# Kernel optimization log

Measured on AMD Instinct MI355X. Metric: run time of the kernel, lower is better.

Reference implementation:

```python
import jax, jax.numpy as jnp
import numpy as np

N = 8000      # num_nodes
U = 64        # num_units
D = 2         # input_dim
K = 2         # max_diffusion_step
E = 64000     # edges per support
B = 32        # batch
F = D + U     # concat feature size = 66
M = 2 * K + 1 # num_matrices = 5


def setup_inputs() -> dict:
    key = jax.random.key(0)
    ks = jax.random.split(key, 10)
    return {
        "inputs": jax.random.normal(ks[0], (B, N * D), dtype=jnp.float32),
        "hx": jax.random.normal(ks[1], (B, N * U), dtype=jnp.float32),
        "row0": jax.random.randint(ks[2], (E,), 0, N, dtype=jnp.int32),
        "col0": jax.random.randint(ks[3], (E,), 0, N, dtype=jnp.int32),
        "val0": jax.random.uniform(ks[4], (E,), dtype=jnp.float32) / 8.0,
        "row1": jax.random.randint(ks[5], (E,), 0, N, dtype=jnp.int32),
        "col1": jax.random.randint(ks[6], (E,), 0, N, dtype=jnp.int32),
        "val1": jax.random.uniform(ks[7], (E,), dtype=jnp.float32) / 8.0,
        "W_ru": jax.random.normal(ks[8], (F * M, 2 * U), dtype=jnp.float32) * 0.05,
        "b_ru": jnp.ones((2 * U,), dtype=jnp.float32),  # bias_start=1.0
        "W_c": jax.random.normal(ks[9], (F * M, U), dtype=jnp.float32) * 0.05,
        "b_c": jnp.zeros((U,), dtype=jnp.float32),       # bias_start=0.0
    }


def _spmm(row, col, val, x):
    # y[r] += val_e * x[c]  for each edge e=(r,c); x: [N, F*B]
    return jax.ops.segment_sum(val[:, None] * x[col], row, num_segments=N)


def _gconv(inputs, state, W, b, supports, output_size):
    # inputs: [B, N*D_in], state: [B, N*D_st]
    x = jnp.concatenate([inputs.reshape(B, N, -1), state.reshape(B, N, -1)], axis=2)  # [B,N,F]
    f = x.shape[2]
    x0 = x.transpose(1, 2, 0).reshape(N, f * B)  # [N, F*B]
    xs = [x0]
    for (row, col, val) in supports:
        x1 = _spmm(row, col, val, x0)
        xs.append(x1)
        xk_1, xk_2 = x1, x0
        for _ in range(2, K + 1):
            x2 = 2.0 * _spmm(row, col, val, xk_1) - xk_2
            xs.append(x2)
            xk_1, xk_2 = x2, xk_1
    m = len(xs)
    # [M,N,F,B] -> [B,N,F,M] -> [B*N, F*M]
    xc = jnp.stack(xs).reshape(m, N, f, B).transpose(3, 1, 2, 0).reshape(B * N, f * m)
    out = xc @ W + b
    return out.reshape(B, N * output_size)


def reference(inputs, hx, row0, col0, val0, row1, col1, val1, W_ru, b_ru, W_c, b_c):
    supports = ((row0, col0, val0), (row1, col1, val1))
    # reset/update gates via graph convolution
    value = jax.nn.sigmoid(_gconv(inputs, hx, W_ru, b_ru, supports, 2 * U))
    value = value.reshape(B, N, 2 * U)
    r = value[..., :U].reshape(B, N * U)
    u = value[..., U:].reshape(B, N * U)
    c = jnp.tanh(_gconv(inputs, r * hx, W_c, b_c, supports, U))
    new_state = u * hx + (1.0 - u) * c
    return new_state
```

## Files before the change

kernel.cpp:

```cpp
#include <hip/hip_runtime.h>
#include <stdint.h>

#define NN 8000
#define UU 64
#define EE 64000
#define BB 32
#define NB 256000
#define HXS 512000

typedef __attribute__((ext_vector_type(8))) __bf16 bf16x8;
typedef __attribute__((ext_vector_type(4))) float f32x4;
typedef __attribute__((ext_vector_type(4))) unsigned int u32x4;

__device__ __forceinline__ unsigned short f2bf(float f){
  unsigned int u = __builtin_bit_cast(unsigned int, f);
  u += 0x7fffu + ((u >> 16) & 1u);
  return (unsigned short)(u >> 16);
}
__device__ __forceinline__ unsigned int pack2(float a, float b){
  return (unsigned int)f2bf(a) | ((unsigned int)f2bf(b) << 16);
}
__device__ __forceinline__ float bflo(unsigned int w){ return __builtin_bit_cast(float, w << 16); }
__device__ __forceinline__ float bfhi(unsigned int w){ return __builtin_bit_cast(float, w & 0xffff0000u); }
__device__ __forceinline__ float bfu(unsigned short v){ return __builtin_bit_cast(float, (unsigned int)v << 16); }

__device__ __forceinline__ void acc8(float* a, float v, uint4 q){
  a[0]+=v*bflo(q.x); a[1]+=v*bfhi(q.x); a[2]+=v*bflo(q.y); a[3]+=v*bfhi(q.y);
  a[4]+=v*bflo(q.z); a[5]+=v*bfhi(q.z); a[6]+=v*bflo(q.w); a[7]+=v*bfhi(q.w);
}

__device__ __forceinline__ void stage16(const unsigned short* g, unsigned short* ldsbase){
  __builtin_amdgcn_global_load_lds((const __attribute__((address_space(1))) void*)g,
                                   (__attribute__((address_space(3))) void*)ldsbase, 16, 0, 0);
}

__global__ void k_hist(const int* __restrict__ r0, const int* __restrict__ r1, int* __restrict__ cnt){
  int i = blockIdx.x * 256 + threadIdx.x;
  if (i < 2*EE){
    int s = (i >= EE);
    int r = s ? r1[i - EE] : r0[i];
    atomicAdd(&cnt[s*NN + r], 1);
  }
}

__global__ __launch_bounds__(1024) void k_scan(const int* __restrict__ cnt, int* __restrict__ row_ptr, int* __restrict__ rp_work){
  int sup = blockIdx.x;
  const int* c = cnt + sup*NN;
  __shared__ int part[1024];
  int t = threadIdx.x;
  int loc[8]; int s = 0;
  #pragma unroll
  for (int j=0;j<8;j++){ int idx=t*8+j; int v = (idx<NN)? c[idx]:0; loc[j]=s; s+=v; }
  part[t]=s; __syncthreads();
  for (int o=1;o<1024;o<<=1){
    int v = (t>=o)? part[t-o]:0;
    __syncthreads();
    part[t]+=v;
    __syncthreads();
  }
  int pre = (t>0)? part[t-1]:0;
  #pragma unroll
  for (int j=0;j<8;j++){ int idx=t*8+j; if(idx<NN){ int e=pre+loc[j]; row_ptr[sup*(NN+1)+idx]=e; rp_work[sup*NN+idx]=e; } }
  if (t==1023) row_ptr[sup*(NN+1)+NN] = part[1023];
}

__global__ void k_scatter(const int* __restrict__ r0, const int* __restrict__ c0, const float* __restrict__ v0,
                          const int* __restrict__ r1, const int* __restrict__ c1, const float* __restrict__ v1,
                          int* __restrict__ rp_work, int* __restrict__ col_s, float* __restrict__ val_s){
  int i = blockIdx.x * 256 + threadIdx.x;
  if (i < 2*EE){
    int s = (i >= EE);
    int e = s ? i - EE : i;
    int r  = s ? r1[e] : r0[e];
    int cc = s ? c1[e] : c0[e];
    float vv = s ? v1[e] : v0[e];
    int pos = atomicAdd(&rp_work[s*NN + r], 1);
    col_s[s*EE + pos] = cc;
    val_s[s*EE + pos] = vv;
  }
}

__global__ void k_wpack(const float* __restrict__ W_ru, const float* __restrict__ W_c,
                        unsigned short* __restrict__ Wru_t, unsigned short* __restrict__ Wc_t){
  int i = blockIdx.x * 256 + threadIdx.x;
  int k = i / 192; int oo = i % 192;
  const float* W; int ld, NC; unsigned short* dst; int c;
  if (oo < 128){ W = W_ru; ld = 128; NC = 128; dst = Wru_t; c = oo; }
  else         { W = W_c;  ld = 64;  NC = 64;  dst = Wc_t;  c = oo - 128; }
  int o = 4*(c & 15) + ((c >> 4) & 3);
  int wcol = (c >= 64) ? 64 + o : o;
  float v = 0.f;
  if (k < 330){
    int m, fb;
    if (k < 320){ m = k >> 6; fb = (2 + (k & 63)) * 5; }
    else        { int j = k - 320; m = j >> 1; fb = (j & 1) * 5; }
    if      (m==0) v = W[(fb+0)*ld+wcol] - W[(fb+2)*ld+wcol] - W[(fb+4)*ld+wcol];
    else if (m==1) v = W[(fb+1)*ld+wcol];
    else if (m==2) v = 2.f*W[(fb+2)*ld+wcol];
    else if (m==3) v = W[(fb+3)*ld+wcol];
    else           v = 2.f*W[(fb+4)*ld+wcol];
  }
  int dstoff;
  if (k < 320) dstoff = (k>>6)*NC*64 + c*64 + (k&63);
  else         dstoff = 320*NC + c*32 + (k-320);
  dst[dstoff] = f2bf(v);
}

__global__ void k_x0(const float* __restrict__ inputs, const float* __restrict__ hx,
                     uint4* __restrict__ xs0q, unsigned int* __restrict__ xi0){
  int n = blockIdx.x, t = threadIdx.x;
  int b = t >> 3, ug = t & 7;
  const float4 h0 = *(const float4*)(hx + (size_t)b*HXS + n*64 + ug*8);
  const float4 h1 = *(const float4*)(hx + (size_t)b*HXS + n*64 + ug*8 + 4);
  uint4 o;
  o.x = pack2(h0.x, h0.y); o.y = pack2(h0.z, h0.w);
  o.z = pack2(h1.x, h1.y); o.w = pack2(h1.z, h1.w);
  xs0q[(size_t)(b>>1)*(NN*16) + (size_t)n*16 + (b&1)*8 + ug] = o;
  if (t < 32){
    int bb = t;
    const float2 g = *(const float2*)(inputs + (size_t)bb*(NN*2) + n*2);
    xi0[(((size_t)(bb>>2)*NN) + n)*4 + (bb&3)] = pack2(g.x, g.y);
  }
}

template<bool WITH_IN, bool NTDST>
__global__ void k_spmm(const int* __restrict__ row_ptr, const int* __restrict__ col_s, const float* __restrict__ val_s,
                       uint4* xs4, uint4* xi4,
                       int srcA, int dstA, int srcB, int dstB){
  int bid = blockIdx.x;
  if (WITH_IN && bid >= 16000){
    int b2 = bid - 16000;
    int s = b2 & 7, supi = (b2 >> 3) & 1, chunk = b2 >> 4;
    int n = chunk*256 + threadIdx.x;
    if (n >= NN) return;
    int msrc = supi ? srcB : srcA, mdst = supi ? dstB : dstA;
    size_t sb = (size_t)(msrc*8 + s)*NN, db = (size_t)(mdst*8 + s)*NN;
    int beg = row_ptr[supi*(NN+1)+n], end = row_ptr[supi*(NN+1)+n+1];
    const int* cs = col_s + supi*EE; const float* vs = val_s + supi*EE;
    float ai[8] = {0.f,0.f,0.f,0.f,0.f,0.f,0.f,0.f};
    for (int e = beg; e < end; ++e){
      int c = cs[e]; float v = vs[e];
      uint4 qi = xi4[sb + c];
      acc8(ai, v, qi);
    }
    uint4 oi;
    oi.x = pack2(ai[0],ai[1]); oi.y = pack2(ai[2],ai[3]); oi.z = pack2(ai[4],ai[5]); oi.w = pack2(ai[6],ai[7]);
    if (NTDST){
      u32x4 ov = {oi.x, oi.y, oi.z, oi.w};
      __builtin_nontemporal_store(ov, (u32x4*)&xi4[db + n]);
    } else xi4[db + n] = oi;
    return;
  }
  int xcd = bid & 7;
  int seq = bid >> 3;
  int supi = (seq >= 1000) ? 1 : 0;
  int seq2 = seq - supi*1000;
  int slice = (seq2 < 500) ? xcd : (xcd + 8);
  int group = (seq2 < 500) ? seq2 : (seq2 - 500);
  int sub = threadIdx.x >> 4, lane = threadIdx.x & 15;
  int n = group*16 + sub;
  int msrc = supi ? srcB : srcA, mdst = supi ? dstB : dstA;
  size_t sS = (size_t)msrc*(NN*256) + (size_t)slice*(NN*16);
  size_t dS = (size_t)mdst*(NN*256) + (size_t)slice*(NN*16);
  int beg = row_ptr[supi*(NN+1)+n], end = row_ptr[supi*(NN+1)+n+1];
  const int* cs = col_s + supi*EE;
  const float* vs = val_s + supi*EE;

  float a[8] = {0.f,0.f,0.f,0.f,0.f,0.f,0.f,0.f};
  int e = beg;
  for (; e + 4 <= end; e += 4){
    int c0=cs[e], c1=cs[e+1], c2=cs[e+2], c3=cs[e+3];
    float v0=vs[e], v1=vs[e+1], v2=vs[e+2], v3=vs[e+3];
    uint4 q0 = xs4[sS + (size_t)c0*16 + lane];
    uint4 q1 = xs4[sS + (size_t)c1*16 + lane];
    uint4 q2 = xs4[sS + (size_t)c2*16 + lane];
    uint4 q3 = xs4[sS + (size_t)c3*16 + lane];
    acc8(a, v0, q0); acc8(a, v1, q1); acc8(a, v2, q2); acc8(a, v3, q3);
  }
  for (; e < end; ++e){
    int c = cs[e]; float v = vs[e];
    uint4 q = xs4[sS + (size_t)c*16 + lane];
    acc8(a, v, q);
  }
  uint4 o;
  o.x = pack2(a[0],a[1]); o.y = pack2(a[2],a[3]); o.z = pack2(a[4],a[5]); o.w = pack2(a[6],a[7]);
  if (NTDST){
    u32x4 ov = {o.x, o.y, o.z, o.w};
    __builtin_nontemporal_store(ov, (u32x4*)&xs4[dS + (size_t)n*16 + lane]);
  } else xs4[dS + (size_t)n*16 + lane] = o;
}

template<int NCOL, bool IS_RU>
__global__ __launch_bounds__(256, 3) void k_gemm(unsigned short* xsS,
                                                 const unsigned int* __restrict__ xsI,
                                                 const unsigned short* __restrict__ Wp,
                                                 const float* __restrict__ bias,
                                                 const float* __restrict__ hx,
                                                 float* cout,
                                                 unsigned short* ubuf){
  constexpr int CF = NCOL / 16;
  __shared__ unsigned short Bl[2][NCOL*64];
  __shared__ unsigned short Bt[NCOL*32];
  const int t = threadIdx.x;
  const int wv = t >> 6;
  const int l = t & 63;
  const int lr = l & 15;
  const int lg = l >> 4;
  const int R0 = blockIdx.x * 128;

  auto stageB = [&](int m, int buf){
    #pragma unroll
    for (int i=0;i<NCOL*8/256;i++){
      int g = t + i*256;
      int rr = g >> 3, c = g & 7;
      const unsigned short* gp = Wp + (size_t)(m*NCOL + rr)*64 + ((c ^ (rr&7)) << 3);
      stage16(gp, &Bl[buf][(size_t)(i*256 + wv*64)*8]);
    }
  };

  size_t abase[2];
  #pragma unroll
  for (int rf=0; rf<2; rf++){
    int row = R0 + wv*32 + rf*16 + lr;
    int n = row >> 5, b = row & 31;
    abase[rf] = (size_t)(b>>1)*(NN*128) + (size_t)n*128 + (b&1)*64;
  }
  auto loadA = [&](int m, uint4* dst){
    #pragma unroll
    for (int ks=0; ks<2; ks++)
      #pragma unroll
      for (int rf=0; rf<2; rf++)
        dst[ks*2+rf] = *(const uint4*)(xsS + (size_t)m*(NN*2048) + abase[rf] + ks*32 + lg*8);
  };

  uint4 aC[4], aN[4];
  loadA(0, aC);
  uint4 aT[2];
  #pragma unroll
  for (int rf=0; rf<2; rf++){
    int row = R0 + wv*32 + rf*16 + lr;
    int n = row >> 5, b = row & 31;
    size_t ib = (((size_t)(b>>2))*NN + n)*4 + (b&3);
    unsigned int q0=0u,q1=0u,q2=0u,q3=0u;
    if (lg == 0){
      q0 = xsI[ib];
      q1 = xsI[(size_t)8*NN*4 + ib];
      q2 = xsI[(size_t)16*NN*4 + ib];
      q3 = xsI[(size_t)24*NN*4 + ib];
    } else if (lg == 1){
      q0 = xsI[(size_t)32*NN*4 + ib];
    }
    uint4 qq; qq.x=q0; qq.y=q1; qq.z=q2; qq.w=q3;
    aT[rf] = qq;
  }
  stageB(0, 0);
  {
    #pragma unroll
    for (int i=0;i<NCOL*4/256;i++){
      int g = t + i*256;
      int rr = g >> 2, c = g & 3;
      const unsigned short* gp = Wp + (size_t)320*NCOL + rr*32 + ((c ^ (rr&3)) << 3);
      stage16(gp, &Bt[(size_t)(i*256 + wv*64)*8]);
    }
  }
  __syncthreads();

  f32x4 acc[2][CF];
  const f32x4 zero = {0.f,0.f,0.f,0.f};
  #pragma unroll
  for (int rf=0; rf<2; rf++)
    #pragma unroll
    for (int cf=0; cf<CF; cf++) acc[rf][cf] = zero;

  #pragma unroll
  for (int m=0; m<5; m++){
    int cur = m & 1;
    if (m < 4){
      stageB(m+1, cur^1);
      loadA(m+1, aN);
    }
    #pragma unroll
    for (int ks=0; ks<2; ks++){
      #pragma unroll
      for (int cf=0; cf<CF; cf++){
        int col = cf*16 + lr;
        int chunk = (ks*4 + lg) ^ (col & 7);
        bf16x8 bv = __builtin_bit_cast(bf16x8, *(const uint4*)(&Bl[cur][col*64 + chunk*8]));
        acc[0][cf] = __builtin_amdgcn_mfma_f32_16x16x32_bf16(__builtin_bit_cast(bf16x8, aC[ks*2+0]), bv, acc[0][cf], 0, 0, 0);
        acc[1][cf] = __builtin_amdgcn_mfma_f32_16x16x32_bf16(__builtin_bit_cast(bf16x8, aC[ks*2+1]), bv, acc[1][cf], 0, 0, 0);
      }
    }
    __syncthreads();
    #pragma unroll
    for (int i=0;i<4;i++) aC[i] = aN[i];
  }

  #pragma unroll
  for (int cf=0; cf<CF; cf++){
    int col = cf*16 + lr;
    int chunk = lg ^ (col & 3);
    bf16x8 bv = __builtin_bit_cast(bf16x8, *(const uint4*)(&Bt[col*32 + chunk*8]));
    acc[0][cf] = __builtin_amdgcn_mfma_f32_16x16x32_bf16(__builtin_bit_cast(bf16x8, aT[0]), bv, acc[0][cf], 0, 0, 0);
    acc[1][cf] = __builtin_amdgcn_mfma_f32_16x16x32_bf16(__builtin_bit_cast(bf16x8, aT[1]), bv, acc[1][cf], 0, 0, 0);
  }

  #pragma unroll
  for (int rf=0; rf<2; rf++){
    #pragma unroll
    for (int reg=0; reg<4; reg++){
      int row = R0 + wv*32 + rf*16 + (lg << 2) + reg;
      int n = row >> 5, b = row & 31;
      size_t rowoff = (size_t)b*HXS + (size_t)n*UU;
      size_t slot0 = (size_t)(b>>1)*(NN*128) + (size_t)n*128 + (b&1)*64;
      int o0 = lr << 2;
      if constexpr (IS_RU){
        uint2 hv = *(const uint2*)(xsS + slot0 + o0);
        unsigned short rr4[4], uu4[4];
        #pragma unroll
        for (int cf=0; cf<4; cf++){
          int o = o0 + cf;
          float vr = acc[rf][cf][reg]   + bias[o];
          float vu = acc[rf][cf+4][reg] + bias[64+o];
          float sgr = 1.f/(1.f + __expf(-vr));
          float sgu = 1.f/(1.f + __expf(-vu));
          float h = bfu(((const unsigned short*)&hv)[cf]);
          rr4[cf] = f2bf(sgr * h);
          uu4[cf] = f2bf(sgu);
        }
        *(uint2*)(xsS + slot0 + o0) = *(uint2*)rr4;
        *(uint2*)(ubuf + rowoff + o0) = *(uint2*)uu4;
      } else {
        float4 hv = *(const float4*)(hx + rowoff + o0);
        uint2 uv = *(const uint2*)(ubuf + rowoff + o0);
        float4 ov;
        #pragma unroll
        for (int cf=0; cf<4; cf++){
          float cc = tanhf(acc[rf][cf][reg] + bias[o0+cf]);
          float uu = bfu(((const unsigned short*)&uv)[cf]);
          float h  = ((const float*)&hv)[cf];
          ((float*)&ov)[cf] = uu*h + (1.f - uu)*cc;
        }
        *(float4*)(cout + rowoff + o0) = ov;
      }
    }
  }
}

extern "C" void kernel_launch(void* const* d_in, const int* in_sizes, int n_in,
                              void* d_out, int out_size, void* d_ws, size_t ws_size,
                              hipStream_t stream){
  const float* inputs = (const float*)d_in[0];
  const float* hx     = (const float*)d_in[1];
  const int*   row0   = (const int*)d_in[2];
  const int*   col0   = (const int*)d_in[3];
  const float* val0   = (const float*)d_in[4];
  const int*   row1   = (const int*)d_in[5];
  const int*   col1   = (const int*)d_in[6];
  const float* val1   = (const float*)d_in[7];
  const float* W_ru   = (const float*)d_in[8];
  const float* b_ru   = (const float*)d_in[9];
  const float* W_c    = (const float*)d_in[10];
  const float* b_c    = (const float*)d_in[11];
  float* out = (float*)d_out;

  char* ws = (char*)d_ws;
  size_t off = 0;
  auto alloc = [&](size_t bytes) -> void* {
    void* p = ws + off;
    off += (bytes + 255) & ~(size_t)255;
    return p;
  };
  unsigned short* xsS   = (unsigned short*)alloc((size_t)5*NN*2048*2);
  unsigned int*   xsI   = (unsigned int*)  alloc((size_t)5*8*NN*16);
  unsigned short* u_buf = (unsigned short*)alloc((size_t)NB*64*2);
  unsigned short* Wru_t = (unsigned short*)alloc((size_t)128*352*2);
  unsigned short* Wc_t  = (unsigned short*)alloc((size_t)64*352*2);
  int*   row_ptr = (int*)  alloc(2*(NN+1)*4);
  int*   col_s   = (int*)  alloc(2*EE*4);
  float* val_s   = (float*)alloc(2*EE*4);
  int*   cnt     = (int*)  alloc(2*NN*4);
  int*   rp_work = (int*)  alloc(2*NN*4);
  (void)ws_size; (void)in_sizes; (void)n_in; (void)out_size;

  hipMemsetAsync(cnt, 0, 2*NN*4, stream);
  k_hist<<<(2*EE + 255)/256, 256, 0, stream>>>(row0, row1, cnt);
  k_scan<<<2, 1024, 0, stream>>>(cnt, row_ptr, rp_work);
  k_scatter<<<(2*EE + 255)/256, 256, 0, stream>>>(row0, col0, val0, row1, col1, val1, rp_work, col_s, val_s);
  k_wpack<<<(352*192)/256, 256, 0, stream>>>(W_ru, W_c, Wru_t, Wc_t);
  k_x0<<<NN, 256, 0, stream>>>(inputs, hx, (uint4*)xsS, (unsigned int*)xsI);

  uint4* xs4 = (uint4*)xsS;
  uint4* xi4 = (uint4*)xsI;

  k_spmm<true , false><<<16512, 256, 0, stream>>>(row_ptr, col_s, val_s, xs4, xi4, 0, 1, 0, 3);
  k_spmm<true , true ><<<16512, 256, 0, stream>>>(row_ptr, col_s, val_s, xs4, xi4, 1, 2, 3, 4);
  k_gemm<128, true><<<2000, 256, 0, stream>>>(xsS, xsI, Wru_t, b_ru, hx, nullptr, u_buf);

  k_spmm<false, false><<<16000, 256, 0, stream>>>(row_ptr, col_s, val_s, xs4, xi4, 0, 1, 0, 3);
  k_spmm<false, true ><<<16000, 256, 0, stream>>>(row_ptr, col_s, val_s, xs4, xi4, 1, 2, 3, 4);
  k_gemm<64, false><<<2000, 256, 0, stream>>>(xsS, xsI, Wc_t, b_c, hx, out, u_buf);
}
```

Baseline: 393.9 us.

## Preload all GEMM weights into LDS and stream A tiles via async LDS loads

The GEMM kernel now stages every weight slice (all five diffusion matrices plus the input tail) into shared memory up front. It streams activation fragments through a per-wave double-buffered LDS area using direct global-to-LDS loads with explicit vmcnt waits, replacing per-iteration block barriers. SpMM kernels drop the template flag and always write outputs with nontemporal stores. The larger shared-memory footprint lowers occupancy, and nontemporal stores on intermediate hops may hurt cache reuse by the following hop.

```diff
diff --git a/kernel.cpp b/kernel.cpp
--- a/kernel.cpp
+++ b/kernel.cpp
@@ -32,6 +32,11 @@
 __device__ __forceinline__ void stage16(const unsigned short* g, unsigned short* ldsbase){
   __builtin_amdgcn_global_load_lds((const __attribute__((address_space(1))) void*)g,
                                    (__attribute__((address_space(3))) void*)ldsbase, 16, 0, 0);
+}
+
+__device__ __forceinline__ void ntstore16(uint4 v, uint4* p){
+  u32x4 ov = {v.x, v.y, v.z, v.w};
+  __builtin_nontemporal_store(ov, (u32x4*)p);
 }
 
 __global__ void k_hist(const int* __restrict__ r0, const int* __restrict__ r1, int* __restrict__ cnt){
@@ -123,7 +128,7 @@
   }
 }
 
-template<bool WITH_IN, bool NTDST>
+template<bool WITH_IN>
 __global__ void k_spmm(const int* __restrict__ row_ptr, const int* __restrict__ col_s, const float* __restrict__ val_s,
                        uint4* xs4, uint4* xi4,
                        int srcA, int dstA, int srcB, int dstB){
@@ -145,10 +150,7 @@
     }
     uint4 oi;
     oi.x = pack2(ai[0],ai[1]); oi.y = pack2(ai[2],ai[3]); oi.z = pack2(ai[4],ai[5]); oi.w = pack2(ai[6],ai[7]);
-    if (NTDST){
-      u32x4 ov = {oi.x, oi.y, oi.z, oi.w};
-      __builtin_nontemporal_store(ov, (u32x4*)&xi4[db + n]);
-    } else xi4[db + n] = oi;
+    ntstore16(oi, &xi4[db + n]);
     return;
   }
   int xcd = bid & 7;
@@ -184,23 +186,24 @@
   }
   uint4 o;
   o.x = pack2(a[0],a[1]); o.y = pack2(a[2],a[3]); o.z = pack2(a[4],a[5]); o.w = pack2(a[6],a[7]);
-  if (NTDST){
-    u32x4 ov = {o.x, o.y, o.z, o.w};
-    __builtin_nontemporal_store(ov, (u32x4*)&xs4[dS + (size_t)n*16 + lane]);
-  } else xs4[dS + (size_t)n*16 + lane] = o;
+  ntstore16(o, &xs4[dS + (size_t)n*16 + lane]);
 }
 
 template<int NCOL, bool IS_RU>
-__global__ __launch_bounds__(256, 3) void k_gemm(unsigned short* xsS,
-                                                 const unsigned int* __restrict__ xsI,
-                                                 const unsigned short* __restrict__ Wp,
-                                                 const float* __restrict__ bias,
-                                                 const float* __restrict__ hx,
-                                                 float* cout,
-                                                 unsigned short* ubuf){
+__global__ __launch_bounds__(256) void k_gemm(unsigned short* xsS,
+                                              const unsigned int* __restrict__ xsI,
+                                              const unsigned short* __restrict__ Wp,
+                                              const float* __restrict__ bias,
+                                              const float* __restrict__ hx,
+                                              float* cout,
+                                              unsigned short* ubuf){
   constexpr int CF = NCOL / 16;
-  __shared__ unsigned short Bl[2][NCOL*64];
-  __shared__ unsigned short Bt[NCOL*32];
+  constexpr int BMAIN = 5*NCOL*64;
+  constexpr int BLD  = (5*NCOL*64/8)/256;
+  constexpr int BLDT = (NCOL*32/8)/256;
+  __shared__ unsigned short Bs[NCOL*352];
+  __shared__ unsigned short As[2][4][4][512];
+
   const int t = threadIdx.x;
   const int wv = t >> 6;
   const int l = t & 63;
@@ -208,16 +211,6 @@
   const int lg = l >> 4;
   const int R0 = blockIdx.x * 128;
 
-  auto stageB = [&](int m, int buf){
-    #pragma unroll
-    for (int i=0;i<NCOL*8/256;i++){
-      int g = t + i*256;
-      int rr = g >> 3, c = g & 7;
-      const unsigned short* gp = Wp + (size_t)(m*NCOL + rr)*64 + ((c ^ (rr&7)) << 3);
-      stage16(gp, &Bl[buf][(size_t)(i*256 + wv*64)*8]);
-    }
-  };
-
   size_t abase[2];
   #pragma unroll
   for (int rf=0; rf<2; rf++){
@@ -225,16 +218,7 @@
     int n = row >> 5, b = row & 31;
     abase[rf] = (size_t)(b>>1)*(NN*128) + (size_t)n*128 + (b&1)*64;
   }
-  auto loadA = [&](int m, uint4* dst){
-    #pragma unroll
-    for (int ks=0; ks<2; ks++)
-      #pragma unroll
-      for (int rf=0; rf<2; rf++)
-        dst[ks*2+rf] = *(const uint4*)(xsS + (size_t)m*(NN*2048) + abase[rf] + ks*32 + lg*8);
-  };
-
-  uint4 aC[4], aN[4];
-  loadA(0, aC);
+
   uint4 aT[2];
   #pragma unroll
   for (int rf=0; rf<2; rf++){
@@ -253,17 +237,30 @@
     uint4 qq; qq.x=q0; qq.y=q1; qq.z=q2; qq.w=q3;
     aT[rf] = qq;
   }
-  stageB(0, 0);
-  {
+  #pragma unroll
+  for (int i=0;i<BLD;i++){
+    int g = t + i*256;
+    int rr = g >> 3, c = g & 7;
+    const unsigned short* gp = Wp + (size_t)rr*64 + ((c ^ (rr&7)) << 3);
+    stage16(gp, &Bs[(size_t)(i*256 + wv*64)*8]);
+  }
+  #pragma unroll
+  for (int i=0;i<BLDT;i++){
+    int g = t + i*256;
+    int rr = g >> 2, c = g & 3;
+    const unsigned short* gp = Wp + (size_t)BMAIN + rr*32 + ((c ^ (rr&3)) << 3);
+    stage16(gp, &Bs[BMAIN + (size_t)(i*256 + wv*64)*8]);
+  }
+  auto stageA = [&](int m, int set){
     #pragma unroll
-    for (int i=0;i<NCOL*4/256;i++){
-      int g = t + i*256;
-      int rr = g >> 2, c = g & 3;
-      const unsigned short* gp = Wp + (size_t)320*NCOL + rr*32 + ((c ^ (rr&3)) << 3);
-      stage16(gp, &Bt[(size_t)(i*256 + wv*64)*8]);
+    for (int f=0; f<4; f++){
+      int ks = f >> 1, rf = f & 1;
+      const unsigned short* gp = xsS + (size_t)m*(NN*2048) + abase[rf] + ks*32 + lg*8;
+      stage16(gp, &As[set][wv][f][0]);
     }
-  }
-  __syncthreads();
+  };
+  stageA(0, 0);
+  __builtin_amdgcn_sched_barrier(0);
 
   f32x4 acc[2][CF];
   const f32x4 zero = {0.f,0.f,0.f,0.f};
@@ -274,32 +271,36 @@
 
   #pragma unroll
   for (int m=0; m<5; m++){
-    int cur = m & 1;
-    if (m < 4){
-      stageB(m+1, cur^1);
-      loadA(m+1, aN);
-    }
+    if (m < 4) stageA(m+1, (m+1)&1);
+    if (m == 4) { asm volatile("s_waitcnt vmcnt(0)" ::: "memory"); }
+    else        { asm volatile("s_waitcnt vmcnt(4)" ::: "memory"); }
+    if (m == 0) __builtin_amdgcn_s_barrier();
+    __builtin_amdgcn_sched_barrier(0);
+    bf16x8 af[2][2];
+    #pragma unroll
+    for (int ks=0; ks<2; ks++)
+      #pragma unroll
+      for (int rf=0; rf<2; rf++)
+        af[ks][rf] = __builtin_bit_cast(bf16x8, *(const uint4*)(&As[m&1][wv][ks*2+rf][l*8]));
+    const unsigned short* Bm = Bs + m*NCOL*64;
     #pragma unroll
     for (int ks=0; ks<2; ks++){
       #pragma unroll
       for (int cf=0; cf<CF; cf++){
         int col = cf*16 + lr;
         int chunk = (ks*4 + lg) ^ (col & 7);
-        bf16x8 bv = __builtin_bit_cast(bf16x8, *(const uint4*)(&Bl[cur][col*64 + chunk*8]));
-        acc[0][cf] = __builtin_amdgcn_mfma_f32_16x16x32_bf16(__builtin_bit_cast(bf16x8, aC[ks*2+0]), bv, acc[0][cf], 0, 0, 0);
-        acc[1][cf] = __builtin_amdgcn_mfma_f32_16x16x32_bf16(__builtin_bit_cast(bf16x8, aC[ks*2+1]), bv, acc[1][cf], 0, 0, 0);
+        bf16x8 bv = __builtin_bit_cast(bf16x8, *(const uint4*)(Bm + col*64 + chunk*8));
+        acc[0][cf] = __builtin_amdgcn_mfma_f32_16x16x32_bf16(af[ks][0], bv, acc[0][cf], 0, 0, 0);
+        acc[1][cf] = __builtin_amdgcn_mfma_f32_16x16x32_bf16(af[ks][1], bv, acc[1][cf], 0, 0, 0);
       }
     }
-    __syncthreads();
-    #pragma unroll
-    for (int i=0;i<4;i++) aC[i] = aN[i];
   }
 
   #pragma unroll
   for (int cf=0; cf<CF; cf++){
     int col = cf*16 + lr;
     int chunk = lg ^ (col & 3);
-    bf16x8 bv = __builtin_bit_cast(bf16x8, *(const uint4*)(&Bt[col*32 + chunk*8]));
+    bf16x8 bv = __builtin_bit_cast(bf16x8, *(const uint4*)(&Bs[BMAIN + col*32 + chunk*8]));
     acc[0][cf] = __builtin_amdgcn_mfma_f32_16x16x32_bf16(__builtin_bit_cast(bf16x8, aT[0]), bv, acc[0][cf], 0, 0, 0);
     acc[1][cf] = __builtin_amdgcn_mfma_f32_16x16x32_bf16(__builtin_bit_cast(bf16x8, aT[1]), bv, acc[1][cf], 0, 0, 0);
   }
@@ -392,11 +393,11 @@
   uint4* xs4 = (uint4*)xsS;
   uint4* xi4 = (uint4*)xsI;
 
-  k_spmm<true , false><<<16512, 256, 0, stream>>>(row_ptr, col_s, val_s, xs4, xi4, 0, 1, 0, 3);
-  k_spmm<true , true ><<<16512, 256, 0, stream>>>(row_ptr, col_s, val_s, xs4, xi4, 1, 2, 3, 4);
+  k_spmm<true ><<<16512, 256, 0, stream>>>(row_ptr, col_s, val_s, xs4, xi4, 0, 1, 0, 3);
+  k_spmm<true ><<<16512, 256, 0, stream>>>(row_ptr, col_s, val_s, xs4, xi4, 1, 2, 3, 4);
   k_gemm<128, true><<<2000, 256, 0, stream>>>(xsS, xsI, Wru_t, b_ru, hx, nullptr, u_buf);
 
-  k_spmm<false, false><<<16000, 256, 0, stream>>>(row_ptr, col_s, val_s, xs4, xi4, 0, 1, 0, 3);
-  k_spmm<false, true ><<<16000, 256, 0, stream>>>(row_ptr, col_s, val_s, xs4, xi4, 1, 2, 3, 4);
+  k_spmm<false><<<16000, 256, 0, stream>>>(row_ptr, col_s, val_s, xs4, xi4, 0, 1, 0, 3);
+  k_spmm<false><<<16000, 256, 0, stream>>>(row_ptr, col_s, val_s, xs4, xi4, 1, 2, 3, 4);
   k_gemm<64, false><<<2000, 256, 0, stream>>>(xsS, xsI, Wc_t, b_c, hx, out, u_buf);
 }
```

Measured after the change: 437.4 us. 1.11x slower.
